# Kernel optimization log

Hardware: AMD Instinct MI355X
Metric: run time of the kernel (lower is better)

The kernel has to match this reference:

```python
import jax, jax.numpy as jnp
import numpy as np


def _mlp(x, W1, b1, W2, b2):
    # x: (B, M, T); torch MLPLayer: transpose(1,2) -> Linear -> Linear -> LeakyReLU -> transpose back
    h = jnp.einsum('bmt,hm->bht', x, W1) + b1[None, :, None]   # (B, H, T)
    y = jnp.einsum('bht,oh->bot', h, W2) + b2[None, :, None]   # (B, M, T)
    return jax.nn.leaky_relu(y, negative_slope=0.01)


def _calc_attn(q, k, v):
    # q: (B, M, Tq), k: (B, M, Tk), v: (B, M, Tk)
    Tq = q.shape[-1]
    qk = jnp.einsum('bmq,bmk->bqk', q, k)                       # (B, Tq, Tk)
    eye = jnp.eye(Tq, dtype=qk.dtype)                           # broadcasts: (Tq,Tq) or (1,1)
    logits = jnp.exp(qk - qk * eye / jnp.sqrt(jnp.asarray(Tq, qk.dtype)))
    scores = jax.nn.softmax(logits, axis=-1)
    return jnp.einsum('bqk,bmk->bmq', scores, v)                # (B, M, Tq)


def setup_inputs() -> dict:
    key = jax.random.key(0)
    B, M, T, H = 16, 128, 2048, 512
    ks = jax.random.split(key, 14)
    s = 0.02
    inp = {
        'pattern': jax.random.normal(ks[0], (B, M, T), jnp.float32),
        'value': jax.random.normal(ks[1], (B, M, T), jnp.float32),
        'kernel_size': 33,
    }
    names = ['q', 'k', 'o']
    for i, n in enumerate(names):
        inp['W%s1' % n] = jax.random.normal(ks[2 + 4 * i], (H, M), jnp.float32) * s
        inp['b%s1' % n] = jax.random.normal(ks[3 + 4 * i], (H,), jnp.float32) * s
        inp['W%s2' % n] = jax.random.normal(ks[4 + 4 * i], (M, H), jnp.float32) * s
        inp['b%s2' % n] = jax.random.normal(ks[5 + 4 * i], (M,), jnp.float32) * s
    return inp


def reference(pattern, value, kernel_size, Wq1, bq1, Wq2, bq2, Wk1, bk1, Wk2, bk2, Wo1, bo1, Wo2, bo2):
    query = _mlp(pattern, Wq1, bq1, Wq2, bq2)
    key = _mlp(pattern, Wk1, bk1, Wk2, bk2)
    # full (internal) attention
    attn_in = _calc_attn(query, key, value)                     # (B, M, T)
    rep_in = _mlp(attn_in, Wo1, bo1, Wo2, bo2)
    # windowed (external) attention
    T = query.shape[-1]
    cu = (kernel_size - 1) // 2
    q_w = query[..., T - 1 - cu : T - cu]                       # (B, M, 1)
    k_w = key[..., kernel_size - cu - 1 : T - cu - 2]           # (B, M, T-k-1)
    v_w = value[..., kernel_size : T - 1]                       # (B, M, T-k-1)
    attn_ex = _calc_attn(q_w, k_w, v_w)                         # (B, M, 1)
    rep_ex = _mlp(attn_ex, Wo1, bo1, Wo2, bo2)
    return jnp.concatenate([rep_in, rep_ex], axis=-1)           # (B, M, T+1)
```

## Files before the change

### kernel.cpp

```cpp
#include <hip/hip_runtime.h>
#include <hip/hip_bf16.h>
#include <math.h>

#define B_    16
#define M_    128
#define T_    2048
#define H_    512
#define TOUT_ 2049

typedef unsigned short u16;
typedef unsigned int   u32;
typedef __bf16 bf16x8 __attribute__((ext_vector_type(8)));
typedef float  f32x16 __attribute__((ext_vector_type(16)));
typedef float  f32x4  __attribute__((ext_vector_type(4)));
typedef u32    u32x4  __attribute__((ext_vector_type(4)));
typedef u32    u32x2  __attribute__((ext_vector_type(2)));

#define A_OFF     0
#define C_OFF     16384
#define MEAN_OFF  16896
#define AQKBF_OFF 19200
#define AOBF_OFF  35584
#define QT_OFF    43776
#define KT_OFF    (43776 + 2097152)
#define VB_OFF    (43776 + 2 * 2097152)

static __device__ __forceinline__ u16 f2bf(float f) {
  u32 u = __float_as_uint(f);
  u = (u + 0x7FFFu + ((u >> 16) & 1u)) >> 16;
  return (u16)u;
}
static __device__ __forceinline__ u32 pk2(float lo, float hi) {
  __hip_bfloat162 h = __float22bfloat162_rn(float2{lo, hi});
  u32 r;
  __builtin_memcpy(&r, &h, 4);
  return r;
}
static __device__ __forceinline__ bf16x8 ldfrag(const u16* p) {
  return __builtin_bit_cast(bf16x8, *(const u32x4*)p);
}
static __device__ __forceinline__ float ex2(float x) {
#if __has_builtin(__builtin_amdgcn_exp2f)
  return __builtin_amdgcn_exp2f(x);
#else
  return exp2f(x);
#endif
}

__global__ __launch_bounds__(128) void fuse_weights_all(
    const float* __restrict__ W1q, const float* __restrict__ b1q,
    const float* __restrict__ W2q, const float* __restrict__ b2q,
    const float* __restrict__ W1k, const float* __restrict__ b1k,
    const float* __restrict__ W2k, const float* __restrict__ b2k,
    const float* __restrict__ W1o, const float* __restrict__ b1o,
    const float* __restrict__ W2o, const float* __restrict__ b2o,
    float* __restrict__ A, float* __restrict__ c,
    u16* __restrict__ Aqk_bf, u16* __restrict__ Ao_bf) {
  __shared__ float w2row[H_];
  int which = blockIdx.x >> 7;
  int o = blockIdx.x & 127;
  const float* W1 = which == 0 ? W1q : which == 1 ? W1k : W1o;
  const float* b1 = which == 0 ? b1q : which == 1 ? b1k : b1o;
  const float* W2 = which == 0 ? W2q : which == 1 ? W2k : W2o;
  const float* b2 = which == 0 ? b2q : which == 1 ? b2k : b2o;
  int m = threadIdx.x;
  for (int h = m; h < H_; h += 128) w2row[h] = W2[o * H_ + h];
  __syncthreads();
  float acc = 0.f;
#pragma unroll 8
  for (int h = 0; h < H_; ++h) acc = fmaf(w2row[h], W1[h * M_ + m], acc);
  u16 ab = f2bf(acc);
  if (which == 0)      Aqk_bf[o * 128 + m] = ab;
  else if (which == 1) Aqk_bf[(128 + o) * 128 + m] = ab;
  else               { Ao_bf[o * 128 + m] = ab; A[o * M_ + m] = acc; }
  if (m < 64) {
    float cc = 0.f;
    for (int h = m; h < H_; h += 64) cc = fmaf(w2row[h], b1[h], cc);
#pragma unroll
    for (int off = 32; off > 0; off >>= 1) cc += __shfl_down(cc, off, 64);
    if (m == 0) c[which * 128 + o] = cc + b2[o];
  }
}

#define XS 68

__global__ __launch_bounds__(256) void prep_kernel(
    const float* __restrict__ pattern, const u16* __restrict__ Aqk_bf,
    const float* __restrict__ cqk, u16* __restrict__ qT, u16* __restrict__ kT,
    const float* __restrict__ value, u16* __restrict__ vb,
    float* __restrict__ meanv) {
  __shared__ alignas(16) float xsf[128 * XS];
  int bx = blockIdx.x;
  int tid = threadIdx.x;

  if (bx >= 512) {
    int bm = bx - 512;
    float* red = xsf;
    const float* row = value + (size_t)bm * T_;
    int i0 = tid * 8;
    float4 a = *(const float4*)(row + i0);
    float4 bq = *(const float4*)(row + i0 + 4);
    u32x4 o = {pk2(a.x, a.y), pk2(a.z, a.w), pk2(bq.x, bq.y), pk2(bq.z, bq.w)};
    *(u32x4*)&vb[(size_t)bm * T_ + i0] = o;
    float vals[8] = {a.x, a.y, a.z, a.w, bq.x, bq.y, bq.z, bq.w};
    float s = 0.f;
#pragma unroll
    for (int j = 0; j < 8; ++j) {
      int idx = i0 + j;
      if (idx >= 33 && idx < T_ - 1) s += vals[j];
    }
    red[tid] = s;
    __syncthreads();
    for (int st = 128; st > 0; st >>= 1) {
      if (tid < st) red[tid] += red[tid + st];
      __syncthreads();
    }
    if (tid == 0) meanv[bm] = red[0] * (1.f / 2014.f);
    return;
  }

  int b = bx >> 5;
  int t0 = (bx & 31) * 64;
  int lane = tid & 63;
  int wv = tid >> 6;
  int l31 = lane & 31;
  int lh8 = (lane >> 5) * 8;

  bf16x8 afr[2][8];
#pragma unroll
  for (int i = 0; i < 2; ++i) {
    const u16* ap = Aqk_bf + ((2 * wv + i) * 32 + l31) * 128 + lh8;
#pragma unroll
    for (int s = 0; s < 8; ++s) afr[i][s] = ldfrag(ap + 16 * s);
  }

#pragma unroll
  for (int rep = 0; rep < 8; ++rep) {
    int m = rep * 16 + (tid >> 4);
    int tc = (tid & 15) * 4;
    float4 v = *(const float4*)&pattern[(size_t)(b * M_ + m) * T_ + t0 + tc];
    *(float4*)&xsf[m * XS + tc] = v;
  }
  __syncthreads();

  bf16x8 bfr[2][8];
#pragma unroll
  for (int tt = 0; tt < 2; ++tt) {
#pragma unroll
    for (int s = 0; s < 8; ++s) {
      float v0 = xsf[(s * 16 + lh8 + 0) * XS + tt * 32 + l31];
      float v1 = xsf[(s * 16 + lh8 + 1) * XS + tt * 32 + l31];
      float v2 = xsf[(s * 16 + lh8 + 2) * XS + tt * 32 + l31];
      float v3 = xsf[(s * 16 + lh8 + 3) * XS + tt * 32 + l31];
      float v4 = xsf[(s * 16 + lh8 + 4) * XS + tt * 32 + l31];
      float v5 = xsf[(s * 16 + lh8 + 5) * XS + tt * 32 + l31];
      float v6 = xsf[(s * 16 + lh8 + 6) * XS + tt * 32 + l31];
      float v7 = xsf[(s * 16 + lh8 + 7) * XS + tt * 32 + l31];
      u32x4 p = {pk2(v0, v1), pk2(v2, v3), pk2(v4, v5), pk2(v6, v7)};
      bfr[tt][s] = __builtin_bit_cast(bf16x8, p);
    }
  }
  __syncthreads();

  u16* obuf = (u16*)xsf;
#pragma unroll
  for (int tt = 0; tt < 2; ++tt) {
#pragma unroll
    for (int i = 0; i < 2; ++i) {
      f32x16 acc;
#pragma unroll
      for (int r = 0; r < 16; ++r) acc[r] = 0.f;
#pragma unroll
      for (int s = 0; s < 8; ++s)
        acc = __builtin_amdgcn_mfma_f32_32x32x16_bf16(afr[i][s], bfr[tt][s], acc, 0, 0, 0);
      int ot = 2 * wv + i;
      int t = tt * 32 + l31;
      float sc = (ot < 4) ? 1.44269504f : 1.0f;
#pragma unroll
      for (int r = 0; r < 16; ++r) {
        int orow = (r & 3) + 8 * (r >> 2) + 4 * (lane >> 5);
        float v = acc[r] + cqk[ot * 32 + orow];
        v = v > 0.f ? v : 0.01f * v;
        obuf[t * 258 + ot * 32 + orow] = f2bf(v * sc);
      }
    }
  }
  __syncthreads();

  const u32* ob32 = (const u32*)obuf;
#pragma unroll
  for (int g = 0; g < 8; ++g) {
    int G = wv * 8 + g;
    int mat = G >> 4;
    int t = (G & 15) * 4 + (lane >> 4);
    int og2 = lane & 15;
    int wbase = t * 129 + mat * 64 + og2 * 4;
    u32x4 vv = {ob32[wbase], ob32[wbase + 1], ob32[wbase + 2], ob32[wbase + 3]};
    u32* dst = (u32*)((mat ? kT : qT) + ((size_t)(b * T_ + t0 + t)) * 128) + og2 * 4;
    *(u32x4*)dst = vv;
  }
}

#define QSTR 136
#define VSTR 136
#define KTILE 128
#define NKT  (T_ / KTILE)
#define CINIT 0.52876637f

__global__ __launch_bounds__(512, 2) void attn_mfma_kernel(
    const u16* __restrict__ qT, const u16* __restrict__ kT,
    const u16* __restrict__ vB, const u16* __restrict__ Ao_bf,
    const float* __restrict__ co, const float* __restrict__ Aofp,
    const float* __restrict__ meanv, float* __restrict__ out) {
  extern __shared__ u16 smem[];
  u16* ks0 = smem;
  u16* ks1 = ks0 + 128 * QSTR;
  u16* vs0 = ks1 + 128 * QSTR;
  u16* vs1 = vs0 + 128 * VSTR;
  float* dls  = (float*)(vs1 + 128 * VSTR);
  float* pbuf = (float*)ks0;
  u16*   ptbuf = vs0;

  int b = blockIdx.y;
  int q0 = blockIdx.x * 128;
  int tid = threadIdx.x;
  int lane = tid & 63;
  int wv = tid >> 6;
  int l31 = lane & 31;
  int h = lane >> 5;
  int lh8 = h * 8;
  int qt = wv & 3;
  int kh = wv >> 2;

  const u16* gkb = kT + (size_t)b * T_ * 128;
  const u16* gvb = vB + (size_t)b * M_ * T_;
  int kr = tid >> 4, kc = (tid & 15) * 8;

  bf16x8 qfrag[8];
  {
    const u16* qrow = qT + (size_t)(b * T_ + q0 + qt * 32 + l31) * 128 + lh8;
#pragma unroll
    for (int s = 0; s < 8; ++s) qfrag[s] = ldfrag(qrow + s * 16);
  }

  u32x4 kreg[4], vreg[4];
#pragma unroll
  for (int it = 0; it < 4; ++it) {
    kreg[it] = *(const u32x4*)&gkb[(size_t)(it * 32 + kr) * 128 + kc];
    vreg[it] = *(const u32x4*)&gvb[(size_t)(it * 32 + kr) * T_ + kc];
  }
#pragma unroll
  for (int it = 0; it < 4; ++it) {
    *(u32x4*)&ks0[(it * 32 + kr) * QSTR + kc] = kreg[it];
    *(u32x4*)&vs0[(it * 32 + kr) * VSTR + kc] = vreg[it];
  }
#pragma unroll
  for (int it = 0; it < 4; ++it) {
    kreg[it] = *(const u32x4*)&gkb[(size_t)(KTILE + it * 32 + kr) * 128 + kc];
    vreg[it] = *(const u32x4*)&gvb[(size_t)(it * 32 + kr) * T_ + KTILE + kc];
  }

  f32x16 pacc[4];
  float den = 0.f;
#pragma unroll
  for (int i = 0; i < 16; ++i) {
    pacc[0][i] = 0.f; pacc[1][i] = 0.f; pacc[2][i] = 0.f; pacc[3][i] = 0.f;
  }

  for (int kt = 0; kt < NKT; ++kt) {
    int k0 = kt * KTILE;
    u16* kcur = (kt & 1) ? ks1 : ks0;
    u16* knxt = (kt & 1) ? ks0 : ks1;
    u16* vcur = (kt & 1) ? vs1 : vs0;
    u16* vnxt = (kt & 1) ? vs0 : vs1;
    __syncthreads();

    f32x16 sacc_a, sacc_b;
#pragma unroll
    for (int i = 0; i < 16; ++i) { sacc_a[i] = CINIT; sacc_b[i] = CINIT; }
    {
      const u16* krowa = &kcur[(kh * 64 + l31) * QSTR + lh8];
      const u16* krowb = krowa + 32 * QSTR;
      __builtin_amdgcn_s_setprio(1);
#pragma unroll
      for (int s = 0; s < 8; ++s) {
        bf16x8 kfa = ldfrag(krowa + s * 16);
        sacc_a = __builtin_amdgcn_mfma_f32_32x32x16_bf16(kfa, qfrag[s], sacc_a, 0, 0, 0);
      }
#pragma unroll
      for (int s = 0; s < 8; ++s) {
        bf16x8 kfb = ldfrag(krowb + s * 16);
        sacc_b = __builtin_amdgcn_mfma_f32_32x32x16_bf16(kfb, qfrag[s], sacc_b, 0, 0, 0);
      }
      __builtin_amdgcn_s_setprio(0);
    }

    if (kt < NKT - 1) {
#pragma unroll
      for (int it = 0; it < 4; ++it) {
        *(u32x4*)&knxt[(it * 32 + kr) * QSTR + kc] = kreg[it];
        *(u32x4*)&vnxt[(it * 32 + kr) * VSTR + kc] = vreg[it];
      }
      int kn = (kt + 2 < NKT) ? (kt + 2) * KTILE : (NKT - 1) * KTILE;
#pragma unroll
      for (int it = 0; it < 4; ++it) {
        kreg[it] = *(const u32x4*)&gkb[(size_t)(kn + it * 32 + kr) * 128 + kc];
        vreg[it] = *(const u32x4*)&gvb[(size_t)(it * 32 + kr) * T_ + kn + kc];
      }
    }

    if (k0 + kh * 64 == q0 + qt * 32) {
#pragma unroll
      for (int r = 0; r < 16; ++r) {
        int row = (r & 3) + 8 * (r >> 2) + 4 * h;
        if (row == l31) sacc_a[r] = fmaf(sacc_a[r], 0.97790291f, 0.01168420f);
      }
    } else if (k0 + kh * 64 + 32 == q0 + qt * 32) {
#pragma unroll
      for (int r = 0; r < 16; ++r) {
        int row = (r & 3) + 8 * (r >> 2) + 4 * h;
        if (row == l31) sacc_b[r] = fmaf(sacc_b[r], 0.97790291f, 0.01168420f);
      }
    }

    {
      float w[16];
#pragma unroll
      for (int r = 0; r < 16; ++r) w[r] = ex2(ex2(sacc_a[r]));
      float d0 = (w[0] + w[1]) + (w[2] + w[3]);
      float d1 = (w[4] + w[5]) + (w[6] + w[7]);
      float d2 = (w[8] + w[9]) + (w[10] + w[11]);
      float d3 = (w[12] + w[13]) + (w[14] + w[15]);
      den += (d0 + d1) + (d2 + d3);
      u32 p00 = pk2(w[0], w[1]),  p01 = pk2(w[2], w[3]);
      u32 p10 = pk2(w[4], w[5]),  p11 = pk2(w[6], w[7]);
      u32 p20 = pk2(w[8], w[9]),  p21 = pk2(w[10], w[11]);
      u32 p30 = pk2(w[12], w[13]), p31 = pk2(w[14], w[15]);
      u32 e0 = __shfl_xor(h ? p00 : p10, 32, 64);
      u32 e1 = __shfl_xor(h ? p01 : p11, 32, 64);
      u32 e2 = __shfl_xor(h ? p20 : p30, 32, 64);
      u32 e3 = __shfl_xor(h ? p21 : p31, 32, 64);
      u32x4 f0 = h ? u32x4{e0, e1, p10, p11} : u32x4{p00, p01, e0, e1};
      u32x4 f1 = h ? u32x4{e2, e3, p30, p31} : u32x4{p20, p21, e2, e3};
      bf16x8 bw0 = __builtin_bit_cast(bf16x8, f0);
      bf16x8 bw1 = __builtin_bit_cast(bf16x8, f1);
      __builtin_amdgcn_s_setprio(1);
#pragma unroll
      for (int mt = 0; mt < 4; ++mt) {
        const u16* vrow = &vcur[(mt * 32 + l31) * VSTR + kh * 64 + lh8];
        bf16x8 vf0 = ldfrag(vrow);
        bf16x8 vf1 = ldfrag(vrow + 16);
        pacc[mt] = __builtin_amdgcn_mfma_f32_32x32x16_bf16(vf0, bw0, pacc[mt], 0, 0, 0);
        pacc[mt] = __builtin_amdgcn_mfma_f32_32x32x16_bf16(vf1, bw1, pacc[mt], 0, 0, 0);
      }
      __builtin_amdgcn_s_setprio(0);
    }
    {
      float w[16];
#pragma unroll
      for (int r = 0; r < 16; ++r) w[r] = ex2(ex2(sacc_b[r]));
      float d0 = (w[0] + w[1]) + (w[2] + w[3]);
      float d1 = (w[4] + w[5]) + (w[6] + w[7]);
      float d2 = (w[8] + w[9]) + (w[10] + w[11]);
      float d3 = (w[12] + w[13]) + (w[14] + w[15]);
      den += (d0 + d1) + (d2 + d3);
      u32 p00 = pk2(w[0], w[1]),  p01 = pk2(w[2], w[3]);
      u32 p10 = pk2(w[4], w[5]),  p11 = pk2(w[6], w[7]);
      u32 p20 = pk2(w[8], w[9]),  p21 = pk2(w[10], w[11]);
      u32 p30 = pk2(w[12], w[13]), p31 = pk2(w[14], w[15]);
      u32 e0 = __shfl_xor(h ? p00 : p10, 32, 64);
      u32 e1 = __shfl_xor(h ? p01 : p11, 32, 64);
      u32 e2 = __shfl_xor(h ? p20 : p30, 32, 64);
      u32 e3 = __shfl_xor(h ? p21 : p31, 32, 64);
      u32x4 f0 = h ? u32x4{e0, e1, p10, p11} : u32x4{p00, p01, e0, e1};
      u32x4 f1 = h ? u32x4{e2, e3, p30, p31} : u32x4{p20, p21, e2, e3};
      bf16x8 bw2 = __builtin_bit_cast(bf16x8, f0);
      bf16x8 bw3 = __builtin_bit_cast(bf16x8, f1);
      __builtin_amdgcn_s_setprio(1);
#pragma unroll
      for (int mt = 0; mt < 4; ++mt) {
        const u16* vrow = &vcur[(mt * 32 + l31) * VSTR + kh * 64 + 32 + lh8];
        bf16x8 vf2 = ldfrag(vrow);
        bf16x8 vf3 = ldfrag(vrow + 16);
        pacc[mt] = __builtin_amdgcn_mfma_f32_32x32x16_bf16(vf2, bw2, pacc[mt], 0, 0, 0);
        pacc[mt] = __builtin_amdgcn_mfma_f32_32x32x16_bf16(vf3, bw3, pacc[mt], 0, 0, 0);
      }
      __builtin_amdgcn_s_setprio(0);
    }
  }

  float dq = den + __shfl_xor(den, 32, 64);

  __syncthreads();

  if (kh == 1) {
#pragma unroll
    for (int mt = 0; mt < 4; ++mt) {
      float* pb = &pbuf[((size_t)(qt * 4 + mt) * 64 + lane) * 16];
#pragma unroll
      for (int g = 0; g < 4; ++g) {
        f32x4 v = {pacc[mt][4 * g], pacc[mt][4 * g + 1],
                   pacc[mt][4 * g + 2], pacc[mt][4 * g + 3]};
        *(f32x4*)(pb + 4 * g) = v;
      }
    }
    if (lane < 32) dls[qt * 32 + lane] = dq;
  }
  __syncthreads();

  if (kh == 0) {
    float rden = 1.f / (dq + dls[qt * 32 + l31]);
#pragma unroll
    for (int mt = 0; mt < 4; ++mt) {
      const float* pb = &pbuf[((size_t)(qt * 4 + mt) * 64 + lane) * 16];
#pragma unroll
      for (int g = 0; g < 4; ++g) {
        f32x4 t = *(const f32x4*)(pb + 4 * g);
        float v0 = (pacc[mt][4 * g + 0] + t[0]) * rden;
        float v1 = (pacc[mt][4 * g + 1] + t[1]) * rden;
        float v2 = (pacc[mt][4 * g + 2] + t[2]) * rden;
        float v3 = (pacc[mt][4 * g + 3] + t[3]) * rden;
        int m0 = mt * 32 + 8 * g + 4 * h;
        u32x2 wp = {pk2(v0, v1), pk2(v2, v3)};
        *(u32x2*)&ptbuf[(qt * 32 + l31) * QSTR + m0] = wp;
      }
    }
  }
  __syncthreads();

  bf16x8 aofr[8];
  {
    const u16* ap = Ao_bf + ((wv & 3) * 32 + l31) * 128 + lh8;
#pragma unroll
    for (int s = 0; s < 8; ++s) aofr[s] = ldfrag(ap + 16 * s);
  }
#pragma unroll
  for (int j = 0; j < 2; ++j) {
    int qt2 = kh * 2 + j;
    bf16x8 pfr[8];
    const u16* pp = &ptbuf[(qt2 * 32 + l31) * QSTR + lh8];
#pragma unroll
    for (int s = 0; s < 8; ++s) pfr[s] = ldfrag(pp + 16 * s);
    f32x16 oacc;
#pragma unroll
    for (int r = 0; r < 16; ++r) oacc[r] = 0.f;
#pragma unroll
    for (int s = 0; s < 8; ++s)
      oacc = __builtin_amdgcn_mfma_f32_32x32x16_bf16(aofr[s], pfr[s], oacc, 0, 0, 0);
#pragma unroll
    for (int r = 0; r < 16; ++r) {
      int orow = (wv & 3) * 32 + (r & 3) + 8 * (r >> 2) + 4 * h;
      float v = oacc[r] + co[orow];
      v = v > 0.f ? v : 0.01f * v;
      out[((size_t)(b * M_ + orow)) * TOUT_ + q0 + qt2 * 32 + l31] = v;
    }
  }

  if (blockIdx.x == 0 && tid < 128) {
    float acc = co[tid];
    const float* mv = meanv + b * 128;
    for (int m = 0; m < 128; ++m) acc = fmaf(Aofp[tid * 128 + m], mv[m], acc);
    acc = acc > 0.f ? acc : 0.01f * acc;
    out[((size_t)(b * M_ + tid)) * TOUT_ + 2048] = acc;
  }
}

extern "C" void kernel_launch(void* const* d_in, const int* in_sizes, int n_in,
                              void* d_out, int out_size, void* d_ws, size_t ws_size,
                              hipStream_t stream) {
  (void)in_sizes; (void)n_in; (void)out_size; (void)ws_size;
  const float* pattern = (const float*)d_in[0];
  const float* value   = (const float*)d_in[1];
  const float* Wq1 = (const float*)d_in[3];
  const float* bq1 = (const float*)d_in[4];
  const float* Wq2 = (const float*)d_in[5];
  const float* bq2 = (const float*)d_in[6];
  const float* Wk1 = (const float*)d_in[7];
  const float* bk1 = (const float*)d_in[8];
  const float* Wk2 = (const float*)d_in[9];
  const float* bk2 = (const float*)d_in[10];
  const float* Wo1 = (const float*)d_in[11];
  const float* bo1 = (const float*)d_in[12];
  const float* Wo2 = (const float*)d_in[13];
  const float* bo2 = (const float*)d_in[14];

  float* ws     = (float*)d_ws;
  float* A      = ws + A_OFF;
  float* c      = ws + C_OFF;
  float* meanv  = ws + MEAN_OFF;
  u16*   Aqk_bf = (u16*)(ws + AQKBF_OFF);
  u16*   Ao_bf  = (u16*)(ws + AOBF_OFF);
  u16*   qT     = (u16*)(ws + QT_OFF);
  u16*   kT     = (u16*)(ws + KT_OFF);
  u16*   vB     = (u16*)(ws + VB_OFF);
  float* out    = (float*)d_out;

  fuse_weights_all<<<384, 128, 0, stream>>>(
      Wq1, bq1, Wq2, bq2, Wk1, bk1, Wk2, bk2, Wo1, bo1, Wo2, bo2,
      A, c, Aqk_bf, Ao_bf);

  prep_kernel<<<512 + B_ * M_, 256, 0, stream>>>(
      pattern, Aqk_bf, c, qT, kT, value, vB, meanv);

  size_t lds_bytes = (size_t)(2 * 128 * QSTR + 2 * 128 * VSTR) * 2 + 128 * 4;
  attn_mfma_kernel<<<dim3(T_ / 128, B_), 512, lds_bytes, stream>>>(
      qT, kT, vB, Ao_bf, c + 256, A, meanv, out);
}
```

Before: 190.1 us.

## Software-pipeline attention loop so QK of tile k overlaps softmax/PV of tile k-1

Restructures the attention main loop into a one-stage software pipeline. Each iteration computes QK MFMAs for the current K tile while doing the exp/pack/PV MFMAs for the previous tile's scores, and the loop runs one extra iteration to drain. The goal is to let the dependent transcendental work overlap with independent matrix ops instead of serialising them. In exchange it adds a second __syncthreads per iteration before the LDS refill, keeps extra score registers live (which may raise VGPR pressure), and drops the s_setprio hints.

After: 193.4 us. Within noise of the previous version (+1.7%).

```diff
diff --git a/kernel.cpp b/kernel.cpp
--- a/kernel.cpp
+++ b/kernel.cpp
@@ -267,35 +267,85 @@
     pacc[0][i] = 0.f; pacc[1][i] = 0.f; pacc[2][i] = 0.f; pacc[3][i] = 0.f;
   }
 
-  for (int kt = 0; kt < NKT; ++kt) {
-    int k0 = kt * KTILE;
+  f32x16 spA, spB;
+
+  for (int kt = 0; kt <= NKT; ++kt) {
     u16* kcur = (kt & 1) ? ks1 : ks0;
     u16* knxt = (kt & 1) ? ks0 : ks1;
-    u16* vcur = (kt & 1) ? vs1 : vs0;
+    u16* vprev = ((kt + 1) & 1) ? vs1 : vs0;
     u16* vnxt = (kt & 1) ? vs0 : vs1;
-    __syncthreads();
-
-    f32x16 sacc_a, sacc_b;
-#pragma unroll
-    for (int i = 0; i < 16; ++i) { sacc_a[i] = CINIT; sacc_b[i] = CINIT; }
-    {
+
+    f32x16 scA, scB;
+    if (kt < NKT) {
+      __syncthreads();
+#pragma unroll
+      for (int i = 0; i < 16; ++i) { scA[i] = CINIT; scB[i] = CINIT; }
       const u16* krowa = &kcur[(kh * 64 + l31) * QSTR + lh8];
       const u16* krowb = krowa + 32 * QSTR;
-      __builtin_amdgcn_s_setprio(1);
 #pragma unroll
       for (int s = 0; s < 8; ++s) {
         bf16x8 kfa = ldfrag(krowa + s * 16);
-        sacc_a = __builtin_amdgcn_mfma_f32_32x32x16_bf16(kfa, qfrag[s], sacc_a, 0, 0, 0);
+        scA = __builtin_amdgcn_mfma_f32_32x32x16_bf16(kfa, qfrag[s], scA, 0, 0, 0);
       }
 #pragma unroll
       for (int s = 0; s < 8; ++s) {
         bf16x8 kfb = ldfrag(krowb + s * 16);
-        sacc_b = __builtin_amdgcn_mfma_f32_32x32x16_bf16(kfb, qfrag[s], sacc_b, 0, 0, 0);
-      }
-      __builtin_amdgcn_s_setprio(0);
+        scB = __builtin_amdgcn_mfma_f32_32x32x16_bf16(kfb, qfrag[s], scB, 0, 0, 0);
+      }
+      int k0 = kt * KTILE;
+      if (k0 + kh * 64 == q0 + qt * 32) {
+#pragma unroll
+        for (int r = 0; r < 16; ++r) {
+          int row = (r & 3) + 8 * (r >> 2) + 4 * h;
+          if (row == l31) scA[r] = fmaf(scA[r], 0.97790291f, 0.01168420f);
+        }
+      } else if (k0 + kh * 64 + 32 == q0 + qt * 32) {
+#pragma unroll
+        for (int r = 0; r < 16; ++r) {
+          int row = (r & 3) + 8 * (r >> 2) + 4 * h;
+          if (row == l31) scB[r] = fmaf(scB[r], 0.97790291f, 0.01168420f);
+        }
+      }
+    }
+
+    if (kt > 0) {
+#pragma unroll
+      for (int half = 0; half < 2; ++half) {
+        const f32x16& sp = half ? spB : spA;
+        int koff = kh * 64 + half * 32;
+        float w[16];
+#pragma unroll
+        for (int r = 0; r < 16; ++r) w[r] = ex2(ex2(sp[r]));
+        float d0 = (w[0] + w[1]) + (w[2] + w[3]);
+        float d1 = (w[4] + w[5]) + (w[6] + w[7]);
+        float d2 = (w[8] + w[9]) + (w[10] + w[11]);
+        float d3 = (w[12] + w[13]) + (w[14] + w[15]);
+        den += (d0 + d1) + (d2 + d3);
+        u32 p00 = pk2(w[0], w[1]),  p01 = pk2(w[2], w[3]);
+        u32 p10 = pk2(w[4], w[5]),  p11 = pk2(w[6], w[7]);
+        u32 p20 = pk2(w[8], w[9]),  p21 = pk2(w[10], w[11]);
+        u32 p30 = pk2(w[12], w[13]), p31 = pk2(w[14], w[15]);
+        u32 e0 = __shfl_xor(h ? p00 : p10, 32, 64);
+        u32 e1 = __shfl_xor(h ? p01 : p11, 32, 64);
+        u32 e2 = __shfl_xor(h ? p20 : p30, 32, 64);
+        u32 e3 = __shfl_xor(h ? p21 : p31, 32, 64);
+        u32x4 f0 = h ? u32x4{e0, e1, p10, p11} : u32x4{p00, p01, e0, e1};
+        u32x4 f1 = h ? u32x4{e2, e3, p30, p31} : u32x4{p20, p21, e2, e3};
+        bf16x8 bw0 = __builtin_bit_cast(bf16x8, f0);
+        bf16x8 bw1 = __builtin_bit_cast(bf16x8, f1);
+#pragma unroll
+        for (int mt = 0; mt < 4; ++mt) {
+          const u16* vrow = &vprev[(mt * 32 + l31) * VSTR + koff + lh8];
+          bf16x8 vf0 = ldfrag(vrow);
+          bf16x8 vf1 = ldfrag(vrow + 16);
+          pacc[mt] = __builtin_amdgcn_mfma_f32_32x32x16_bf16(vf0, bw0, pacc[mt], 0, 0, 0);
+          pacc[mt] = __builtin_amdgcn_mfma_f32_32x32x16_bf16(vf1, bw1, pacc[mt], 0, 0, 0);
+        }
+      }
     }
 
     if (kt < NKT - 1) {
+      __syncthreads();
 #pragma unroll
       for (int it = 0; it < 4; ++it) {
         *(u32x4*)&knxt[(it * 32 + kr) * QSTR + kc] = kreg[it];
@@ -309,84 +359,7 @@
       }
     }
 
-    if (k0 + kh * 64 == q0 + qt * 32) {
-#pragma unroll
-      for (int r = 0; r < 16; ++r) {
-        int row = (r & 3) + 8 * (r >> 2) + 4 * h;
-        if (row == l31) sacc_a[r] = fmaf(sacc_a[r], 0.97790291f, 0.01168420f);
-      }
-    } else if (k0 + kh * 64 + 32 == q0 + qt * 32) {
-#pragma unroll
-      for (int r = 0; r < 16; ++r) {
-        int row = (r & 3) + 8 * (r >> 2) + 4 * h;
-        if (row == l31) sacc_b[r] = fmaf(sacc_b[r], 0.97790291f, 0.01168420f);
-      }
-    }
-
-    {
-      float w[16];
-#pragma unroll
-      for (int r = 0; r < 16; ++r) w[r] = ex2(ex2(sacc_a[r]));
-      float d0 = (w[0] + w[1]) + (w[2] + w[3]);
-      float d1 = (w[4] + w[5]) + (w[6] + w[7]);
-      float d2 = (w[8] + w[9]) + (w[10] + w[11]);
-      float d3 = (w[12] + w[13]) + (w[14] + w[15]);
-      den += (d0 + d1) + (d2 + d3);
-      u32 p00 = pk2(w[0], w[1]),  p01 = pk2(w[2], w[3]);
-      u32 p10 = pk2(w[4], w[5]),  p11 = pk2(w[6], w[7]);
-      u32 p20 = pk2(w[8], w[9]),  p21 = pk2(w[10], w[11]);
-      u32 p30 = pk2(w[12], w[13]), p31 = pk2(w[14], w[15]);
-      u32 e0 = __shfl_xor(h ? p00 : p10, 32, 64);
-      u32 e1 = __shfl_xor(h ? p01 : p11, 32, 64);
-      u32 e2 = __shfl_xor(h ? p20 : p30, 32, 64);
-      u32 e3 = __shfl_xor(h ? p21 : p31, 32, 64);
-      u32x4 f0 = h ? u32x4{e0, e1, p10, p11} : u32x4{p00, p01, e0, e1};
-      u32x4 f1 = h ? u32x4{e2, e3, p30, p31} : u32x4{p20, p21, e2, e3};
-      bf16x8 bw0 = __builtin_bit_cast(bf16x8, f0);
-      bf16x8 bw1 = __builtin_bit_cast(bf16x8, f1);
-      __builtin_amdgcn_s_setprio(1);
-#pragma unroll
-      for (int mt = 0; mt < 4; ++mt) {
-        const u16* vrow = &vcur[(mt * 32 + l31) * VSTR + kh * 64 + lh8];
-        bf16x8 vf0 = ldfrag(vrow);
-        bf16x8 vf1 = ldfrag(vrow + 16);
-        pacc[mt] = __builtin_amdgcn_mfma_f32_32x32x16_bf16(vf0, bw0, pacc[mt], 0, 0, 0);
-        pacc[mt] = __builtin_amdgcn_mfma_f32_32x32x16_bf16(vf1, bw1, pacc[mt], 0, 0, 0);
-      }
-      __builtin_amdgcn_s_setprio(0);
-    }
-    {
-      float w[16];
-#pragma unroll
-      for (int r = 0; r < 16; ++r) w[r] = ex2(ex2(sacc_b[r]));
-      float d0 = (w[0] + w[1]) + (w[2] + w[3]);
-      float d1 = (w[4] + w[5]) + (w[6] + w[7]);
-      float d2 = (w[8] + w[9]) + (w[10] + w[11]);
-      float d3 = (w[12] + w[13]) + (w[14] + w[15]);
-      den += (d0 + d1) + (d2 + d3);
-      u32 p00 = pk2(w[0], w[1]),  p01 = pk2(w[2], w[3]);
-      u32 p10 = pk2(w[4], w[5]),  p11 = pk2(w[6], w[7]);
-      u32 p20 = pk2(w[8], w[9]),  p21 = pk2(w[10], w[11]);
-      u32 p30 = pk2(w[12], w[13]), p31 = pk2(w[14], w[15]);
-      u32 e0 = __shfl_xor(h ? p00 : p10, 32, 64);
-      u32 e1 = __shfl_xor(h ? p01 : p11, 32, 64);
-      u32 e2 = __shfl_xor(h ? p20 : p30, 32, 64);
-      u32 e3 = __shfl_xor(h ? p21 : p31, 32, 64);
-      u32x4 f0 = h ? u32x4{e0, e1, p10, p11} : u32x4{p00, p01, e0, e1};
-      u32x4 f1 = h ? u32x4{e2, e3, p30, p31} : u32x4{p20, p21, e2, e3};
-      bf16x8 bw2 = __builtin_bit_cast(bf16x8, f0);
-      bf16x8 bw3 = __builtin_bit_cast(bf16x8, f1);
-      __builtin_amdgcn_s_setprio(1);
-#pragma unroll
-      for (int mt = 0; mt < 4; ++mt) {
-        const u16* vrow = &vcur[(mt * 32 + l31) * VSTR + kh * 64 + 32 + lh8];
-        bf16x8 vf2 = ldfrag(vrow);
-        bf16x8 vf3 = ldfrag(vrow + 16);
-        pacc[mt] = __builtin_amdgcn_mfma_f32_32x32x16_bf16(vf2, bw2, pacc[mt], 0, 0, 0);
-        pacc[mt] = __builtin_amdgcn_mfma_f32_32x32x16_bf16(vf3, bw3, pacc[mt], 0, 0, 0);
-      }
-      __builtin_amdgcn_s_setprio(0);
-    }
+    if (kt < NKT) { spA = scA; spB = scB; }
   }
 
   float dq = den + __shfl_xor(den, 32, 64);
```

## Pre-swizzle Q/K/V into MFMA fragment order and load tiles directly into LDS

Applied to the files above, without the earlier changes.

Q, K and V are now written by the prep kernels in a blocked layout that matches the MFMA fragment order, so the attention kernel can copy K/V tiles with global_load_lds straight into LDS, skipping register staging and padded strides. The attention kernel is repartitioned: each wave now covers two query subtiles against a 32-key slice, sharing K fragments across two MFMAs. It then combines four partial accumulators in a multi-step LDS reduction. The value conversion moves from prep_kernel into the weight-fusion kernel. LDS use rises to about 130 KB, which may limit occupancy, and the longer reduction epilogue adds extra syncs.

After: 204.7 us. 1.08x slower.

```diff
diff --git a/kernel.cpp b/kernel.cpp
--- a/kernel.cpp
+++ b/kernel.cpp
@@ -46,6 +46,11 @@
   return exp2f(x);
 #endif
 }
+static __device__ __forceinline__ void g2l16(const u16* g, u16* l) {
+  __builtin_amdgcn_global_load_lds(
+      (const __attribute__((address_space(1))) u32*)(const void*)g,
+      (__attribute__((address_space(3))) u32*)(void*)l, 16, 0, 0);
+}
 
 __global__ __launch_bounds__(128) void fuse_weights_all(
     const float* __restrict__ W1q, const float* __restrict__ b1q,
@@ -55,15 +60,59 @@
     const float* __restrict__ W1o, const float* __restrict__ b1o,
     const float* __restrict__ W2o, const float* __restrict__ b2o,
     float* __restrict__ A, float* __restrict__ c,
-    u16* __restrict__ Aqk_bf, u16* __restrict__ Ao_bf) {
+    u16* __restrict__ Aqk_bf, u16* __restrict__ Ao_bf,
+    const float* __restrict__ value, u16* __restrict__ vb,
+    float* __restrict__ meanv) {
   __shared__ float w2row[H_];
+  int tid = threadIdx.x;
+
+  if (blockIdx.x >= 384) {
+    int bm = blockIdx.x - 384;
+    int b2 = bm >> 7, m = bm & 127;
+    int mt2 = m >> 5, m31 = m & 31;
+    float* red = w2row;
+    const float* row = value + (size_t)bm * T_;
+    int i0 = tid * 16;
+    float4 a0 = *(const float4*)(row + i0);
+    float4 a1 = *(const float4*)(row + i0 + 4);
+    float4 a2 = *(const float4*)(row + i0 + 8);
+    float4 a3 = *(const float4*)(row + i0 + 12);
+    u32x4 o0 = {pk2(a0.x, a0.y), pk2(a0.z, a0.w), pk2(a1.x, a1.y), pk2(a1.z, a1.w)};
+    u32x4 o1 = {pk2(a2.x, a2.y), pk2(a2.z, a2.w), pk2(a3.x, a3.y), pk2(a3.z, a3.w)};
+#pragma unroll
+    for (int cc = 0; cc < 2; ++cc) {
+      int t8 = i0 + cc * 8;
+      int tb = t8 >> 5, tw = t8 & 31;
+      int s2 = tw >> 4, hb2 = (tw >> 3) & 1;
+      size_t off = ((size_t)((b2 * 64 + tb) * 8 + mt2 * 2 + s2)) * 512
+                 + (hb2 * 32 + m31) * 8;
+      *(u32x4*)&vb[off] = cc ? o1 : o0;
+    }
+    float vals[16] = {a0.x, a0.y, a0.z, a0.w, a1.x, a1.y, a1.z, a1.w,
+                      a2.x, a2.y, a2.z, a2.w, a3.x, a3.y, a3.z, a3.w};
+    float s = 0.f;
+#pragma unroll
+    for (int j = 0; j < 16; ++j) {
+      int idx = i0 + j;
+      if (idx >= 33 && idx < T_ - 1) s += vals[j];
+    }
+    red[tid] = s;
+    __syncthreads();
+    for (int st = 64; st > 0; st >>= 1) {
+      if (tid < st) red[tid] += red[tid + st];
+      __syncthreads();
+    }
+    if (tid == 0) meanv[bm] = red[0] * (1.f / 2014.f);
+    return;
+  }
+
   int which = blockIdx.x >> 7;
   int o = blockIdx.x & 127;
   const float* W1 = which == 0 ? W1q : which == 1 ? W1k : W1o;
   const float* b1 = which == 0 ? b1q : which == 1 ? b1k : b1o;
   const float* W2 = which == 0 ? W2q : which == 1 ? W2k : W2o;
   const float* b2 = which == 0 ? b2q : which == 1 ? b2k : b2o;
-  int m = threadIdx.x;
+  int m = tid;
   for (int h = m; h < H_; h += 128) w2row[h] = W2[o * H_ + h];
   __syncthreads();
   float acc = 0.f;
@@ -86,38 +135,10 @@
 
 __global__ __launch_bounds__(256) void prep_kernel(
     const float* __restrict__ pattern, const u16* __restrict__ Aqk_bf,
-    const float* __restrict__ cqk, u16* __restrict__ qT, u16* __restrict__ kT,
-    const float* __restrict__ value, u16* __restrict__ vb,
-    float* __restrict__ meanv) {
+    const float* __restrict__ cqk, u16* __restrict__ qT, u16* __restrict__ kT) {
   __shared__ alignas(16) float xsf[128 * XS];
   int bx = blockIdx.x;
   int tid = threadIdx.x;
-
-  if (bx >= 512) {
-    int bm = bx - 512;
-    float* red = xsf;
-    const float* row = value + (size_t)bm * T_;
-    int i0 = tid * 8;
-    float4 a = *(const float4*)(row + i0);
-    float4 bq = *(const float4*)(row + i0 + 4);
-    u32x4 o = {pk2(a.x, a.y), pk2(a.z, a.w), pk2(bq.x, bq.y), pk2(bq.z, bq.w)};
-    *(u32x4*)&vb[(size_t)bm * T_ + i0] = o;
-    float vals[8] = {a.x, a.y, a.z, a.w, bq.x, bq.y, bq.z, bq.w};
-    float s = 0.f;
-#pragma unroll
-    for (int j = 0; j < 8; ++j) {
-      int idx = i0 + j;
-      if (idx >= 33 && idx < T_ - 1) s += vals[j];
-    }
-    red[tid] = s;
-    __syncthreads();
-    for (int st = 128; st > 0; st >>= 1) {
-      if (tid < st) red[tid] += red[tid + st];
-      __syncthreads();
-    }
-    if (tid == 0) meanv[bm] = red[0] * (1.f / 2014.f);
-    return;
-  }
 
   int b = bx >> 5;
   int t0 = (bx & 31) * 64;
@@ -196,15 +217,18 @@
     int og2 = lane & 15;
     int wbase = t * 129 + mat * 64 + og2 * 4;
     u32x4 vv = {ob32[wbase], ob32[wbase + 1], ob32[wbase + 2], ob32[wbase + 3]};
-    u32* dst = (u32*)((mat ? kT : qT) + ((size_t)(b * T_ + t0 + t)) * 128) + og2 * 4;
-    *(u32x4*)dst = vv;
-  }
-}
-
-#define QSTR 136
-#define VSTR 136
+    int tg = t0 + t;
+    int kb = tg >> 5, tw = tg & 31;
+    int s = og2 >> 1, hb = og2 & 1;
+    u16* base = mat ? kT : qT;
+    size_t off = (((size_t)b * 64 + kb) * 8 + s) * 512 + (hb * 32 + tw) * 8;
+    *(u32x4*)(base + off) = vv;
+  }
+}
+
 #define KTILE 128
 #define NKT  (T_ / KTILE)
+#define PTSTR 136
 #define CINIT 0.52876637f
 
 __global__ __launch_bounds__(512, 2) void attn_mfma_kernel(
@@ -213,13 +237,13 @@
     const float* __restrict__ co, const float* __restrict__ Aofp,
     const float* __restrict__ meanv, float* __restrict__ out) {
   extern __shared__ u16 smem[];
-  u16* ks0 = smem;
-  u16* ks1 = ks0 + 128 * QSTR;
-  u16* vs0 = ks1 + 128 * QSTR;
-  u16* vs1 = vs0 + 128 * VSTR;
-  float* dls  = (float*)(vs1 + 128 * VSTR);
-  float* pbuf = (float*)ks0;
-  u16*   ptbuf = vs0;
+  u16* kb0 = smem;
+  u16* kb1 = smem + 16384;
+  u16* vb0 = smem + 32768;
+  u16* vb1 = smem + 49152;
+  float* dls = (float*)(smem + 65536);
+  float* pbuf = (float*)smem;
+  u16* ptbuf = smem + 32768;
 
   int b = blockIdx.y;
   int q0 = blockIdx.x * 128;
@@ -228,110 +252,95 @@
   int wv = tid >> 6;
   int l31 = lane & 31;
   int h = lane >> 5;
-  int lh8 = h * 8;
-  int qt = wv & 3;
-  int kh = wv >> 2;
-
-  const u16* gkb = kT + (size_t)b * T_ * 128;
-  const u16* gvb = vB + (size_t)b * M_ * T_;
-  int kr = tid >> 4, kc = (tid & 15) * 8;
-
-  bf16x8 qfrag[8];
+  int qg = wv & 1;
+  int kq = wv >> 1;
+
+  bf16x8 qfA[8], qfB[8];
   {
-    const u16* qrow = qT + (size_t)(b * T_ + q0 + qt * 32 + l31) * 128 + lh8;
-#pragma unroll
-    for (int s = 0; s < 8; ++s) qfrag[s] = ldfrag(qrow + s * 16);
-  }
-
-  u32x4 kreg[4], vreg[4];
-#pragma unroll
-  for (int it = 0; it < 4; ++it) {
-    kreg[it] = *(const u32x4*)&gkb[(size_t)(it * 32 + kr) * 128 + kc];
-    vreg[it] = *(const u32x4*)&gvb[(size_t)(it * 32 + kr) * T_ + kc];
-  }
-#pragma unroll
-  for (int it = 0; it < 4; ++it) {
-    *(u32x4*)&ks0[(it * 32 + kr) * QSTR + kc] = kreg[it];
-    *(u32x4*)&vs0[(it * 32 + kr) * VSTR + kc] = vreg[it];
-  }
-#pragma unroll
-  for (int it = 0; it < 4; ++it) {
-    kreg[it] = *(const u32x4*)&gkb[(size_t)(KTILE + it * 32 + kr) * 128 + kc];
-    vreg[it] = *(const u32x4*)&gvb[(size_t)(it * 32 + kr) * T_ + KTILE + kc];
-  }
-
-  f32x16 pacc[4];
-  float den = 0.f;
-#pragma unroll
-  for (int i = 0; i < 16; ++i) {
-    pacc[0][i] = 0.f; pacc[1][i] = 0.f; pacc[2][i] = 0.f; pacc[3][i] = 0.f;
-  }
+    const u16* qa = qT + (((size_t)b * 64 + (q0 >> 5) + 2 * qg) * 8) * 512 + lane * 8;
+    const u16* qb = qa + 8 * 512;
+#pragma unroll
+    for (int s = 0; s < 8; ++s) {
+      qfA[s] = ldfrag(qa + s * 512);
+      qfB[s] = ldfrag(qb + s * 512);
+    }
+  }
+
+  {
+    const u16* gk = kT + ((size_t)(b * 64) * 8) * 512;
+    const u16* gv = vB + ((size_t)(b * 64) * 8) * 512;
+#pragma unroll
+    for (int c2 = 0; c2 < 4; ++c2) {
+      int ch = wv * 4 + c2;
+      g2l16(gk + (size_t)ch * 512 + lane * 8, kb0 + ch * 512);
+      g2l16(gv + (size_t)ch * 512 + lane * 8, vb0 + ch * 512);
+    }
+  }
+
+  f32x16 pacc[4][2];
+  float den0 = 0.f, den1 = 0.f;
+#pragma unroll
+  for (int mt = 0; mt < 4; ++mt)
+#pragma unroll
+    for (int i = 0; i < 16; ++i) { pacc[mt][0][i] = 0.f; pacc[mt][1][i] = 0.f; }
+
+  __syncthreads();
 
   for (int kt = 0; kt < NKT; ++kt) {
-    int k0 = kt * KTILE;
-    u16* kcur = (kt & 1) ? ks1 : ks0;
-    u16* knxt = (kt & 1) ? ks0 : ks1;
-    u16* vcur = (kt & 1) ? vs1 : vs0;
-    u16* vnxt = (kt & 1) ? vs0 : vs1;
-    __syncthreads();
-
-    f32x16 sacc_a, sacc_b;
-#pragma unroll
-    for (int i = 0; i < 16; ++i) { sacc_a[i] = CINIT; sacc_b[i] = CINIT; }
+    u16* kcur = (kt & 1) ? kb1 : kb0;
+    u16* vcur = (kt & 1) ? vb1 : vb0;
+
+    if (kt + 1 < NKT) {
+      const u16* gk = kT + ((size_t)(b * 64 + (kt + 1) * 4) * 8) * 512;
+      const u16* gv = vB + ((size_t)(b * 64 + (kt + 1) * 4) * 8) * 512;
+      u16* lk = (kt & 1) ? kb0 : kb1;
+      u16* lv = (kt & 1) ? vb0 : vb1;
+#pragma unroll
+      for (int c2 = 0; c2 < 4; ++c2) {
+        int ch = wv * 4 + c2;
+        g2l16(gk + (size_t)ch * 512 + lane * 8, lk + ch * 512);
+        g2l16(gv + (size_t)ch * 512 + lane * 8, lv + ch * 512);
+      }
+    }
+
+    f32x16 sa, sb;
+#pragma unroll
+    for (int i = 0; i < 16; ++i) { sa[i] = CINIT; sb[i] = CINIT; }
     {
-      const u16* krowa = &kcur[(kh * 64 + l31) * QSTR + lh8];
-      const u16* krowb = krowa + 32 * QSTR;
-      __builtin_amdgcn_s_setprio(1);
+      const u16* kl = kcur + (kq * 8) * 512 + lane * 8;
 #pragma unroll
       for (int s = 0; s < 8; ++s) {
-        bf16x8 kfa = ldfrag(krowa + s * 16);
-        sacc_a = __builtin_amdgcn_mfma_f32_32x32x16_bf16(kfa, qfrag[s], sacc_a, 0, 0, 0);
-      }
-#pragma unroll
-      for (int s = 0; s < 8; ++s) {
-        bf16x8 kfb = ldfrag(krowb + s * 16);
-        sacc_b = __builtin_amdgcn_mfma_f32_32x32x16_bf16(kfb, qfrag[s], sacc_b, 0, 0, 0);
-      }
-      __builtin_amdgcn_s_setprio(0);
-    }
-
-    if (kt < NKT - 1) {
-#pragma unroll
-      for (int it = 0; it < 4; ++it) {
-        *(u32x4*)&knxt[(it * 32 + kr) * QSTR + kc] = kreg[it];
-        *(u32x4*)&vnxt[(it * 32 + kr) * VSTR + kc] = vreg[it];
-      }
-      int kn = (kt + 2 < NKT) ? (kt + 2) * KTILE : (NKT - 1) * KTILE;
-#pragma unroll
-      for (int it = 0; it < 4; ++it) {
-        kreg[it] = *(const u32x4*)&gkb[(size_t)(kn + it * 32 + kr) * 128 + kc];
-        vreg[it] = *(const u32x4*)&gvb[(size_t)(it * 32 + kr) * T_ + kn + kc];
-      }
-    }
-
-    if (k0 + kh * 64 == q0 + qt * 32) {
+        bf16x8 kf = ldfrag(kl + s * 512);
+        sa = __builtin_amdgcn_mfma_f32_32x32x16_bf16(kf, qfA[s], sa, 0, 0, 0);
+        sb = __builtin_amdgcn_mfma_f32_32x32x16_bf16(kf, qfB[s], sb, 0, 0, 0);
+      }
+    }
+
+    int kglob = kt * KTILE + kq * 32;
+    if (kglob == q0 + (2 * qg) * 32) {
 #pragma unroll
       for (int r = 0; r < 16; ++r) {
         int row = (r & 3) + 8 * (r >> 2) + 4 * h;
-        if (row == l31) sacc_a[r] = fmaf(sacc_a[r], 0.97790291f, 0.01168420f);
-      }
-    } else if (k0 + kh * 64 + 32 == q0 + qt * 32) {
+        if (row == l31) sa[r] = fmaf(sa[r], 0.97790291f, 0.01168420f);
+      }
+    } else if (kglob == q0 + (2 * qg + 1) * 32) {
 #pragma unroll
       for (int r = 0; r < 16; ++r) {
         int row = (r & 3) + 8 * (r >> 2) + 4 * h;
-        if (row == l31) sacc_b[r] = fmaf(sacc_b[r], 0.97790291f, 0.01168420f);
-      }
-    }
-
+        if (row == l31) sb[r] = fmaf(sb[r], 0.97790291f, 0.01168420f);
+      }
+    }
+
+    bf16x8 bwA0, bwA1, bwB0, bwB1;
     {
       float w[16];
 #pragma unroll
-      for (int r = 0; r < 16; ++r) w[r] = ex2(ex2(sacc_a[r]));
+      for (int r = 0; r < 16; ++r) w[r] = ex2(ex2(sa[r]));
       float d0 = (w[0] + w[1]) + (w[2] + w[3]);
       float d1 = (w[4] + w[5]) + (w[6] + w[7]);
       float d2 = (w[8] + w[9]) + (w[10] + w[11]);
       float d3 = (w[12] + w[13]) + (w[14] + w[15]);
-      den += (d0 + d1) + (d2 + d3);
+      den0 += (d0 + d1) + (d2 + d3);
       u32 p00 = pk2(w[0], w[1]),  p01 = pk2(w[2], w[3]);
       u32 p10 = pk2(w[4], w[5]),  p11 = pk2(w[6], w[7]);
       u32 p20 = pk2(w[8], w[9]),  p21 = pk2(w[10], w[11]);
@@ -342,28 +351,18 @@
       u32 e3 = __shfl_xor(h ? p21 : p31, 32, 64);
       u32x4 f0 = h ? u32x4{e0, e1, p10, p11} : u32x4{p00, p01, e0, e1};
       u32x4 f1 = h ? u32x4{e2, e3, p30, p31} : u32x4{p20, p21, e2, e3};
-      bf16x8 bw0 = __builtin_bit_cast(bf16x8, f0);
-      bf16x8 bw1 = __builtin_bit_cast(bf16x8, f1);
-      __builtin_amdgcn_s_setprio(1);
-#pragma unroll
-      for (int mt = 0; mt < 4; ++mt) {
-        const u16* vrow = &vcur[(mt * 32 + l31) * VSTR + kh * 64 + lh8];
-        bf16x8 vf0 = ldfrag(vrow);
-        bf16x8 vf1 = ldfrag(vrow + 16);
-        pacc[mt] = __builtin_amdgcn_mfma_f32_32x32x16_bf16(vf0, bw0, pacc[mt], 0, 0, 0);
-        pacc[mt] = __builtin_amdgcn_mfma_f32_32x32x16_bf16(vf1, bw1, pacc[mt], 0, 0, 0);
-      }
-      __builtin_amdgcn_s_setprio(0);
+      bwA0 = __builtin_bit_cast(bf16x8, f0);
+      bwA1 = __builtin_bit_cast(bf16x8, f1);
     }
     {
       float w[16];
 #pragma unroll
-      for (int r = 0; r < 16; ++r) w[r] = ex2(ex2(sacc_b[r]));
+      for (int r = 0; r < 16; ++r) w[r] = ex2(ex2(sb[r]));
       float d0 = (w[0] + w[1]) + (w[2] + w[3]);
       float d1 = (w[4] + w[5]) + (w[6] + w[7]);
       float d2 = (w[8] + w[9]) + (w[10] + w[11]);
       float d3 = (w[12] + w[13]) + (w[14] + w[15]);
-      den += (d0 + d1) + (d2 + d3);
+      den1 += (d0 + d1) + (d2 + d3);
       u32 p00 = pk2(w[0], w[1]),  p01 = pk2(w[2], w[3]);
       u32 p10 = pk2(w[4], w[5]),  p11 = pk2(w[6], w[7]);
       u32 p20 = pk2(w[8], w[9]),  p21 = pk2(w[10], w[11]);
@@ -374,60 +373,110 @@
       u32 e3 = __shfl_xor(h ? p21 : p31, 32, 64);
       u32x4 f0 = h ? u32x4{e0, e1, p10, p11} : u32x4{p00, p01, e0, e1};
       u32x4 f1 = h ? u32x4{e2, e3, p30, p31} : u32x4{p20, p21, e2, e3};
-      bf16x8 bw2 = __builtin_bit_cast(bf16x8, f0);
-      bf16x8 bw3 = __builtin_bit_cast(bf16x8, f1);
-      __builtin_amdgcn_s_setprio(1);
+      bwB0 = __builtin_bit_cast(bf16x8, f0);
+      bwB1 = __builtin_bit_cast(bf16x8, f1);
+    }
+
+#pragma unroll
+    for (int mt = 0; mt < 4; ++mt) {
+      const u16* vl = vcur + ((kq * 4 + mt) * 2) * 512 + lane * 8;
+      bf16x8 vf0 = ldfrag(vl);
+      bf16x8 vf1 = ldfrag(vl + 512);
+      pacc[mt][0] = __builtin_amdgcn_mfma_f32_32x32x16_bf16(vf0, bwA0, pacc[mt][0], 0, 0, 0);
+      pacc[mt][0] = __builtin_amdgcn_mfma_f32_32x32x16_bf16(vf1, bwA1, pacc[mt][0], 0, 0, 0);
+      pacc[mt][1] = __builtin_amdgcn_mfma_f32_32x32x16_bf16(vf0, bwB0, pacc[mt][1], 0, 0, 0);
+      pacc[mt][1] = __builtin_amdgcn_mfma_f32_32x32x16_bf16(vf1, bwB1, pacc[mt][1], 0, 0, 0);
+    }
+
+    __syncthreads();
+  }
+
+  float dqA = den0 + __shfl_xor(den0, 32, 64);
+  float dqB = den1 + __shfl_xor(den1, 32, 64);
+  if (lane < 32) {
+    dls[(kq * 4 + 2 * qg + 0) * 32 + l31] = dqA;
+    dls[(kq * 4 + 2 * qg + 1) * 32 + l31] = dqB;
+  }
+  __syncthreads();
+
+  if (kq & 1) {
+    int p = (kq == 3) ? 16 : 0;
+#pragma unroll
+    for (int mt = 0; mt < 4; ++mt)
+#pragma unroll
+      for (int cc = 0; cc < 2; ++cc) {
+        float* pb = &pbuf[(size_t)(p + (qg * 2 + cc) * 4 + mt) * 1024 + lane * 16];
+#pragma unroll
+        for (int g = 0; g < 4; ++g) {
+          f32x4 v = {pacc[mt][cc][4 * g], pacc[mt][cc][4 * g + 1],
+                     pacc[mt][cc][4 * g + 2], pacc[mt][cc][4 * g + 3]};
+          *(f32x4*)(pb + 4 * g) = v;
+        }
+      }
+  }
+  __syncthreads();
+
+  if (!(kq & 1)) {
+    int p = (kq == 2) ? 16 : 0;
+#pragma unroll
+    for (int mt = 0; mt < 4; ++mt)
+#pragma unroll
+      for (int cc = 0; cc < 2; ++cc) {
+        const float* pb = &pbuf[(size_t)(p + (qg * 2 + cc) * 4 + mt) * 1024 + lane * 16];
+#pragma unroll
+        for (int g = 0; g < 4; ++g) {
+          f32x4 t = *(const f32x4*)(pb + 4 * g);
+          pacc[mt][cc][4 * g]     += t[0];
+          pacc[mt][cc][4 * g + 1] += t[1];
+          pacc[mt][cc][4 * g + 2] += t[2];
+          pacc[mt][cc][4 * g + 3] += t[3];
+        }
+      }
+  }
+  __syncthreads();
+
+  if (kq == 2) {
+#pragma unroll
+    for (int mt = 0; mt < 4; ++mt)
+#pragma unroll
+      for (int cc = 0; cc < 2; ++cc) {
+        float* pb = &pbuf[(size_t)((qg * 2 + cc) * 4 + mt) * 1024 + lane * 16];
+#pragma unroll
+        for (int g = 0; g < 4; ++g) {
+          f32x4 v = {pacc[mt][cc][4 * g], pacc[mt][cc][4 * g + 1],
+                     pacc[mt][cc][4 * g + 2], pacc[mt][cc][4 * g + 3]};
+          *(f32x4*)(pb + 4 * g) = v;
+        }
+      }
+  }
+  __syncthreads();
+
+  if (kq == 0) {
+#pragma unroll
+    for (int cc = 0; cc < 2; ++cc) {
+      int qt = 2 * qg + cc;
+      float rden = 1.f / (dls[(0 * 4 + qt) * 32 + l31] + dls[(1 * 4 + qt) * 32 + l31]
+                        + dls[(2 * 4 + qt) * 32 + l31] + dls[(3 * 4 + qt) * 32 + l31]);
 #pragma unroll
       for (int mt = 0; mt < 4; ++mt) {
-        const u16* vrow = &vcur[(mt * 32 + l31) * VSTR + kh * 64 + 32 + lh8];
-        bf16x8 vf2 = ldfrag(vrow);
-        bf16x8 vf3 = ldfrag(vrow + 16);
-        pacc[mt] = __builtin_amdgcn_mfma_f32_32x32x16_bf16(vf2, bw2, pacc[mt], 0, 0, 0);
-        pacc[mt] = __builtin_amdgcn_mfma_f32_32x32x16_bf16(vf3, bw3, pacc[mt], 0, 0, 0);
-      }
-      __builtin_amdgcn_s_setprio(0);
-    }
-  }
-
-  float dq = den + __shfl_xor(den, 32, 64);
-
-  __syncthreads();
-
-  if (kh == 1) {
-#pragma unroll
-    for (int mt = 0; mt < 4; ++mt) {
-      float* pb = &pbuf[((size_t)(qt * 4 + mt) * 64 + lane) * 16];
-#pragma unroll
-      for (int g = 0; g < 4; ++g) {
-        f32x4 v = {pacc[mt][4 * g], pacc[mt][4 * g + 1],
-                   pacc[mt][4 * g + 2], pacc[mt][4 * g + 3]};
-        *(f32x4*)(pb + 4 * g) = v;
-      }
-    }
-    if (lane < 32) dls[qt * 32 + lane] = dq;
-  }
-  __syncthreads();
-
-  if (kh == 0) {
-    float rden = 1.f / (dq + dls[qt * 32 + l31]);
-#pragma unroll
-    for (int mt = 0; mt < 4; ++mt) {
-      const float* pb = &pbuf[((size_t)(qt * 4 + mt) * 64 + lane) * 16];
-#pragma unroll
-      for (int g = 0; g < 4; ++g) {
-        f32x4 t = *(const f32x4*)(pb + 4 * g);
-        float v0 = (pacc[mt][4 * g + 0] + t[0]) * rden;
-        float v1 = (pacc[mt][4 * g + 1] + t[1]) * rden;
-        float v2 = (pacc[mt][4 * g + 2] + t[2]) * rden;
-        float v3 = (pacc[mt][4 * g + 3] + t[3]) * rden;
-        int m0 = mt * 32 + 8 * g + 4 * h;
-        u32x2 wp = {pk2(v0, v1), pk2(v2, v3)};
-        *(u32x2*)&ptbuf[(qt * 32 + l31) * QSTR + m0] = wp;
-      }
-    }
-  }
-  __syncthreads();
-
+        const float* pb = &pbuf[(size_t)((qg * 2 + cc) * 4 + mt) * 1024 + lane * 16];
+#pragma unroll
+        for (int g = 0; g < 4; ++g) {
+          f32x4 t = *(const f32x4*)(pb + 4 * g);
+          float v0 = (pacc[mt][cc][4 * g + 0] + t[0]) * rden;
+          float v1 = (pacc[mt][cc][4 * g + 1] + t[1]) * rden;
+          float v2 = (pacc[mt][cc][4 * g + 2] + t[2]) * rden;
+          float v3 = (pacc[mt][cc][4 * g + 3] + t[3]) * rden;
+          int m0 = mt * 32 + 8 * g + 4 * h;
+          u32x2 wp = {pk2(v0, v1), pk2(v2, v3)};
+          *(u32x2*)&ptbuf[(qt * 32 + l31) * PTSTR + m0] = wp;
+        }
+      }
+    }
+  }
+  __syncthreads();
+
+  int lh8 = h * 8;
   bf16x8 aofr[8];
   {
     const u16* ap = Ao_bf + ((wv & 3) * 32 + l31) * 128 + lh8;
@@ -436,9 +485,9 @@
   }
 #pragma unroll
   for (int j = 0; j < 2; ++j) {
-    int qt2 = kh * 2 + j;
+    int qt2 = (wv >> 2) * 2 + j;
     bf16x8 pfr[8];
-    const u16* pp = &ptbuf[(qt2 * 32 + l31) * QSTR + lh8];
+    const u16* pp = &ptbuf[(qt2 * 32 + l31) * PTSTR + lh8];
 #pragma unroll
     for (int s = 0; s < 8; ++s) pfr[s] = ldfrag(pp + 16 * s);
     f32x16 oacc;
@@ -495,14 +544,13 @@
   u16*   vB     = (u16*)(ws + VB_OFF);
   float* out    = (float*)d_out;
 
-  fuse_weights_all<<<384, 128, 0, stream>>>(
+  fuse_weights_all<<<384 + B_ * M_, 128, 0, stream>>>(
       Wq1, bq1, Wq2, bq2, Wk1, bk1, Wk2, bk2, Wo1, bo1, Wo2, bo2,
-      A, c, Aqk_bf, Ao_bf);
-
-  prep_kernel<<<512 + B_ * M_, 256, 0, stream>>>(
-      pattern, Aqk_bf, c, qT, kT, value, vB, meanv);
-
-  size_t lds_bytes = (size_t)(2 * 128 * QSTR + 2 * 128 * VSTR) * 2 + 128 * 4;
+      A, c, Aqk_bf, Ao_bf, value, vB, meanv);
+
+  prep_kernel<<<512, 256, 0, stream>>>(pattern, Aqk_bf, c, qT, kT);
+
+  size_t lds_bytes = 133120;
   attn_mfma_kernel<<<dim3(T_ / 128, B_), 512, lds_bytes, stream>>>(
       qT, kT, vB, Ao_bf, c + 256, A, meanv, out);
 }
```
